# Kernel optimization log

Hardware: AMD Instinct MI355X
Metric: run time of the kernel (lower is better)

Reference implementation:

```python
import jax, jax.numpy as jnp
import numpy as np

B, T, D_IN, D_HID, D_OUT, N_CAT = 128, 64, 1024, 1024, 1536, 32


def setup_inputs() -> dict:
    key = jax.random.key(0)
    kx, kw1, kw2, kc = jax.random.split(key, 4)
    x = jax.random.normal(kx, (B, T, D_IN), dtype=jnp.float32)
    W1 = 0.02 * jax.random.normal(kw1, (N_CAT, D_IN, D_HID), dtype=jnp.float32)
    b1 = jnp.zeros((N_CAT, D_HID), dtype=jnp.float32)
    W2 = 0.02 * jax.random.normal(kw2, (N_CAT, D_HID, D_OUT), dtype=jnp.float32)
    b2 = jnp.zeros((N_CAT, D_OUT), dtype=jnp.float32)
    cat_ids = jax.random.randint(kc, (B,), 0, N_CAT)
    return {"x": x, "W1": W1, "b1": b1, "W2": W2, "b2": b2, "cat_ids": cat_ids}


def reference(x, W1, b1, W2, b2, cat_ids):
    # CategorySpecificLinear: gather per-sample expert weights, then batched matmul.
    # Layer 1: (B,T,D_in) @ (B,D_in,D_hid) + (B,1,D_hid)
    h = jnp.einsum('btd,bdh->bth', x, W1[cat_ids]) + b1[cat_ids][:, None, :]
    h = jax.nn.relu(h)
    # Layer 2: (B,T,D_hid) @ (B,D_hid,D_out) + (B,1,D_out)
    out = jnp.einsum('bth,bho->bto', h, W2[cat_ids]) + b2[cat_ids][:, None, :]
    return out
```

## Files before the change

kernel.cpp:

```cpp
#include <hip/hip_runtime.h>
#include <hip/hip_bf16.h>
#include <stdint.h>

#define NB    128
#define TT    64
#define KTOT  1024
#define DHID  1024
#define DOUT  1536
#define NCAT  32

#define BK    64
#define TN    128
#define PADR  72

typedef unsigned short u16;
typedef __attribute__((ext_vector_type(8))) short bf16x8;
typedef __attribute__((ext_vector_type(4))) float f32x4;
typedef __attribute__((ext_vector_type(4))) unsigned int uint4v;
typedef __attribute__((ext_vector_type(4))) float float4v;

__device__ __forceinline__ float bf2f(u16 u) {
    unsigned int x = ((unsigned int)u) << 16;
    return __builtin_bit_cast(float, x);
}
__device__ __forceinline__ unsigned int f2bf_u32(float f) {
    unsigned int x = __builtin_bit_cast(unsigned int, f);
    return (x + 0x7FFFu + ((x >> 16) & 1u)) >> 16;
}
__device__ __forceinline__ u16 f2bf(float f) { return (u16)f2bf_u32(f); }

__device__ int g_is_f32;

__global__ void detect_dtype(const unsigned int* __restrict__ xw) {
    if (threadIdx.x == 0 && blockIdx.x == 0) {
        int hits = 0;
        for (int i = 0; i < 256; ++i) {
            unsigned int e = (xw[i] >> 7) & 0xFF;
            hits += (e >= 120 && e <= 132) ? 1 : 0;
        }
        g_is_f32 = (hits < 128) ? 1 : 0;
    }
}

template<int NW, bool RELU, bool A_DYN, bool OUT_DYN>
__global__ __launch_bounds__(256, 4)
void gemm_cat(const void* __restrict__ Ain,
              const void* __restrict__ Win,
              const void* __restrict__ BiasIn,
              void* __restrict__ Cout,
              const int* __restrict__ cat_ids)
{
    constexpr int NT = NW / TN;
    __shared__ u16 As[TT * PADR];
    __shared__ u16 Bs[TN * PADR];

    const bool f32  = (g_is_f32 != 0);
    const bool aF32 = A_DYN && f32;
    const bool oF32 = OUT_DYN && f32;

    const int b   = blockIdx.x / NT;
    const int nt  = blockIdx.x % NT;
    const int cat = cat_ids[b];

    const int tid  = threadIdx.x;
    const int lane = tid & 63;
    const int l16  = lane & 15;
    const int q    = lane >> 4;
    const int wave = tid >> 6;
    const int wm   = wave & 1;
    const int wn   = wave >> 1;

    const size_t aOff = (size_t)b * (TT * KTOT);
    const u16*   Ab16 = (const u16*)Ain + aOff;
    const float* Ab32 = (const float*)Ain + aOff;
    const size_t wOff = (size_t)cat * ((size_t)KTOT * NW) + (size_t)nt * TN;
    const u16*   Wb16 = (const u16*)Win + wOff;
    const float* Wb32 = (const float*)Win + wOff;

    const int ar = tid >> 2;
    const int ac = (tid & 3) * 16;
    const int bn  = tid & 127;
    const int bk0 = tid >> 7;

    f32x4 acc[2][4];
#pragma unroll
    for (int im = 0; im < 2; ++im)
#pragma unroll
        for (int in = 0; in < 4; ++in)
            acc[im][in] = (f32x4){0.f, 0.f, 0.f, 0.f};

    for (int kk = 0; kk < KTOT; kk += BK) {
        if (!aF32) {
            const u16* src = Ab16 + ar * KTOT + kk + ac;
            uint4v v0 = *(const uint4v*)(src);
            uint4v v1 = *(const uint4v*)(src + 8);
            *(uint4v*)&As[ar * PADR + ac]     = v0;
            *(uint4v*)&As[ar * PADR + ac + 8] = v1;
        } else {
            const float* src = Ab32 + ar * KTOT + kk + ac;
            float4v f0 = *(const float4v*)(src);
            float4v f1 = *(const float4v*)(src + 4);
            float4v f2 = *(const float4v*)(src + 8);
            float4v f3 = *(const float4v*)(src + 12);
            uint4v v0, v1;
            v0.x = f2bf_u32(f0.x) | (f2bf_u32(f0.y) << 16);
            v0.y = f2bf_u32(f0.z) | (f2bf_u32(f0.w) << 16);
            v0.z = f2bf_u32(f1.x) | (f2bf_u32(f1.y) << 16);
            v0.w = f2bf_u32(f1.z) | (f2bf_u32(f1.w) << 16);
            v1.x = f2bf_u32(f2.x) | (f2bf_u32(f2.y) << 16);
            v1.y = f2bf_u32(f2.z) | (f2bf_u32(f2.w) << 16);
            v1.z = f2bf_u32(f3.x) | (f2bf_u32(f3.y) << 16);
            v1.w = f2bf_u32(f3.z) | (f2bf_u32(f3.w) << 16);
            *(uint4v*)&As[ar * PADR + ac]     = v0;
            *(uint4v*)&As[ar * PADR + ac + 8] = v1;
        }
#pragma unroll
        for (int i = 0; i < 4; ++i) {
            const int kc = bk0 + i * 2;
            unsigned int s[8];
            if (!f32) {
                const u16* src = Wb16 + (size_t)(kk + kc * 8) * NW + bn;
#pragma unroll
                for (int j = 0; j < 8; ++j) s[j] = src[(size_t)j * NW];
            } else {
                const float* src = Wb32 + (size_t)(kk + kc * 8) * NW + bn;
#pragma unroll
                for (int j = 0; j < 8; ++j) s[j] = f2bf_u32(src[(size_t)j * NW]);
            }
            uint4v v;
            v.x = s[0] | (s[1] << 16);
            v.y = s[2] | (s[3] << 16);
            v.z = s[4] | (s[5] << 16);
            v.w = s[6] | (s[7] << 16);
            *(uint4v*)&Bs[bn * PADR + kc * 8] = v;
        }
        __syncthreads();

#pragma unroll
        for (int s = 0; s < 2; ++s) {
            bf16x8 a[2], bb[4];
#pragma unroll
            for (int im = 0; im < 2; ++im)
                a[im] = *(const bf16x8*)&As[(wm * 32 + im * 16 + l16) * PADR + s * 32 + q * 8];
#pragma unroll
            for (int in = 0; in < 4; ++in)
                bb[in] = *(const bf16x8*)&Bs[(wn * 64 + in * 16 + l16) * PADR + s * 32 + q * 8];
#pragma unroll
            for (int im = 0; im < 2; ++im)
#pragma unroll
                for (int in = 0; in < 4; ++in)
                    acc[im][in] = __builtin_amdgcn_mfma_f32_16x16x32_bf16(
                        a[im], bb[in], acc[im][in], 0, 0, 0);
        }
        __syncthreads();
    }

    const u16*   bias16 = (const u16*)BiasIn + (size_t)cat * NW + nt * TN;
    const float* bias32 = (const float*)BiasIn + (size_t)cat * NW + nt * TN;
    const size_t cOff = (size_t)b * TT * NW + (size_t)nt * TN;
    u16*   C16 = (u16*)Cout + cOff;
    float* C32 = (float*)Cout + cOff;
#pragma unroll
    for (int in = 0; in < 4; ++in) {
        const int ncol = wn * 64 + in * 16 + l16;
        const float bv = f32 ? bias32[ncol] : bf2f(bias16[ncol]);
#pragma unroll
        for (int im = 0; im < 2; ++im) {
#pragma unroll
            for (int r = 0; r < 4; ++r) {
                const int m = wm * 32 + im * 16 + q * 4 + r;
                float v = acc[im][in][r] + bv;
                if (RELU) v = fmaxf(v, 0.f);
                if (oF32) C32[(size_t)m * NW + ncol] = v;
                else      C16[(size_t)m * NW + ncol] = f2bf(v);
            }
        }
    }
}

extern "C" void kernel_launch(void* const* d_in, const int* in_sizes, int n_in,
                              void* d_out, int out_size, void* d_ws, size_t ws_size,
                              hipStream_t stream) {
    const void* x   = d_in[0];
    const void* W1  = d_in[1];
    const void* b1  = d_in[2];
    const void* W2  = d_in[3];
    const void* b2  = d_in[4];
    const int*  cid = (const int*)d_in[5];

    u16* h = (u16*)d_ws;

    detect_dtype<<<1, 64, 0, stream>>>((const unsigned int*)x);
    gemm_cat<DHID, true,  true,  false><<<NB * (DHID / TN), 256, 0, stream>>>(
        x, W1, b1, (void*)h, cid);
    gemm_cat<DOUT, false, false, true ><<<NB * (DOUT / TN), 256, 0, stream>>>(
        (const void*)h, W2, b2, d_out, cid);
}
```

Before: 558.6 us.

## Group samples by category so each weight tile serves up to four batches

Adds a build_groups kernel that sorts samples by category into groups of up to four. A new 512-thread GEMM loads each expert weight tile once and reuses it across all samples in its group. Weight traffic and fp32-to-bf16 conversion per sample drop accordingly. The new path also pre-converts x to bf16 in a separate pass, double-buffers LDS with async global_load_lds for A and register prefetch for W, uses XOR swizzling and a remapped block order, and parallelises dtype detection with a ballot. It needs a larger workspace, launches padded idle blocks, and falls back to the old kernels if the workspace is too small.

```diff
diff --git a/kernel.cpp b/kernel.cpp
--- a/kernel.cpp
+++ b/kernel.cpp
@@ -1,5 +1,4 @@
 #include <hip/hip_runtime.h>
-#include <hip/hip_bf16.h>
 #include <stdint.h>
 
 #define NB    128
@@ -12,6 +11,7 @@
 #define BK    64
 #define TN    128
 #define PADR  72
+#define NGMAX 64
 
 typedef unsigned short u16;
 typedef __attribute__((ext_vector_type(8))) short bf16x8;
@@ -32,13 +32,233 @@
 __device__ int g_is_f32;
 
 __global__ void detect_dtype(const unsigned int* __restrict__ xw) {
-    if (threadIdx.x == 0 && blockIdx.x == 0) {
-        int hits = 0;
-        for (int i = 0; i < 256; ++i) {
-            unsigned int e = (xw[i] >> 7) & 0xFF;
-            hits += (e >= 120 && e <= 132) ? 1 : 0;
-        }
-        g_is_f32 = (hits < 128) ? 1 : 0;
+    const int lane = threadIdx.x;
+    const unsigned int w = xw[lane * 64];
+    const unsigned int e = (w >> 7) & 0xFF;
+    const unsigned long long m = __ballot(e >= 120 && e <= 132);
+    if (lane == 0) g_is_f32 = (__popcll(m) < 32) ? 1 : 0;
+}
+
+__device__ __forceinline__ void gload16(const void* g, void* l) {
+    __builtin_amdgcn_global_load_lds(
+        (const __attribute__((address_space(1))) void*)g,
+        (__attribute__((address_space(3))) void*)l, 16, 0, 0);
+}
+
+__global__ void prep_x(const void* __restrict__ x, u16* __restrict__ xb) {
+    const bool f32 = (g_is_f32 != 0);
+    const size_t base = ((size_t)blockIdx.x * 256 + threadIdx.x) * 8;
+    if (f32) {
+        const float* s = (const float*)x + base;
+        float4v f0 = *(const float4v*)s;
+        float4v f1 = *(const float4v*)(s + 4);
+        uint4v v;
+        v.x = f2bf_u32(f0.x) | (f2bf_u32(f0.y) << 16);
+        v.y = f2bf_u32(f0.z) | (f2bf_u32(f0.w) << 16);
+        v.z = f2bf_u32(f1.x) | (f2bf_u32(f1.y) << 16);
+        v.w = f2bf_u32(f1.z) | (f2bf_u32(f1.w) << 16);
+        *(uint4v*)&xb[base] = v;
+    } else {
+        *(uint4v*)&xb[base] = *(const uint4v*)((const u16*)x + base);
+    }
+}
+
+__global__ void build_groups(const int* __restrict__ cid,
+                             int* __restrict__ gcat, int* __restrict__ gbat) {
+    __shared__ int cl[NB];
+    __shared__ int cnt[NCAT], start[NCAT], gbase[NCAT];
+    __shared__ int sorted[NB];
+    const int t = threadIdx.x;
+    cl[t] = cid[t];
+    if (t < NGMAX) gcat[t] = -1;
+    gbat[t] = -1; gbat[NB + t] = -1;
+    __syncthreads();
+    if (t < NCAT) {
+        int c = 0;
+        for (int i = 0; i < NB; ++i) c += (cl[i] == t) ? 1 : 0;
+        cnt[t] = c;
+    }
+    __syncthreads();
+    if (t == 0) {
+        int s = 0, g = 0;
+        for (int c = 0; c < NCAT; ++c) {
+            start[c] = s; s += cnt[c];
+            gbase[c] = g; g += (cnt[c] + 3) >> 2;
+        }
+    }
+    __syncthreads();
+    {
+        const int myc = cl[t];
+        int r = 0;
+        for (int i = 0; i < t; ++i) r += (cl[i] == myc) ? 1 : 0;
+        sorted[start[myc] + r] = t;
+    }
+    __syncthreads();
+    if (t < NCAT) {
+        const int n = cnt[t], ng = (n + 3) >> 2;
+        for (int j = 0; j < ng; ++j) {
+            const int g = gbase[t] + j;
+            gcat[g] = t;
+            for (int k = 0; k < 4; ++k) {
+                const int idx = j * 4 + k;
+                gbat[g * 4 + k] = (idx < n) ? sorted[start[t] + idx] : -1;
+            }
+        }
+    }
+}
+
+template<int NW, bool RELU, bool OUT_DYN>
+__global__ __launch_bounds__(512, 4)
+void gemm_grp(const u16* __restrict__ A,
+              const void* __restrict__ Win,
+              const void* __restrict__ BiasIn,
+              void* __restrict__ Cout,
+              const int* __restrict__ gcat,
+              const int* __restrict__ gbat)
+{
+    constexpr int NT   = NW / TN;
+    constexpr int NTIL = KTOT / 32;
+    __shared__ __align__(16) u16 As[2][4 * TT * 32];
+    __shared__ __align__(16) u16 Bs[2][TN * 32];
+
+    const int nwg = NGMAX * NT;
+    int bid = blockIdx.x;
+    bid = (bid & 7) * (nwg >> 3) + (bid >> 3);
+    const int g   = bid / NT;
+    const int nt  = bid % NT;
+    const int cat = gcat[g];
+    if (cat < 0) return;
+
+    const bool f32 = (g_is_f32 != 0);
+    const int t    = threadIdx.x;
+    const int wave = t >> 6;
+    const int lane = t & 63;
+    const int l16  = lane & 15;
+    const int q    = lane >> 4;
+    const int wm   = wave & 1;
+    const int wn   = wave >> 1;
+
+    const int bslot[4] = { gbat[g*4+0], gbat[g*4+1], gbat[g*4+2], gbat[g*4+3] };
+
+    const int tt   = t & 255;
+    const int arow = tt >> 2;
+    const int asc  = (((tt & 3) ^ ((tt >> 2) & 3) ^ ((tt >> 4) & 3)) << 3);
+    const int ah   = wave >> 2;
+    const int sA0  = ah, sA1 = 2 + ah;
+    const u16* aG0 = (bslot[sA0] >= 0)
+        ? (A + (size_t)bslot[sA0] * (TT * KTOT) + (size_t)arow * KTOT + asc) : (const u16*)0;
+    const u16* aG1 = (bslot[sA1] >= 0)
+        ? (A + (size_t)bslot[sA1] * (TT * KTOT) + (size_t)arow * KTOT + asc) : (const u16*)0;
+
+    const int bn  = t & 127;
+    const int kc  = t >> 7;
+    const int wch = ((kc ^ (bn & 3) ^ ((bn >> 2) & 3)) << 4);
+    const size_t wOff = (size_t)cat * ((size_t)KTOT * NW) + (size_t)(kc * 8) * NW
+                        + (size_t)nt * TN + bn;
+    const float* w32 = (const float*)Win + wOff;
+    const u16*   w16 = (const u16*)Win + wOff;
+
+    const int CH = ((q ^ (l16 & 3) ^ ((l16 >> 2) & 3)) << 4);
+
+    f32x4 acc[4][2][2];
+#pragma unroll
+    for (int bt = 0; bt < 4; ++bt)
+#pragma unroll
+        for (int im = 0; im < 2; ++im)
+#pragma unroll
+            for (int in = 0; in < 2; ++in)
+                acc[bt][im][in] = (f32x4){0.f, 0.f, 0.f, 0.f};
+
+    unsigned int wr[8];
+
+    auto W_ISSUE = [&](int kk) {
+        if (f32) {
+            const float* ws = w32 + (size_t)kk * NW;
+#pragma unroll
+            for (int j = 0; j < 8; ++j)
+                wr[j] = __builtin_bit_cast(unsigned int, ws[(size_t)j * NW]);
+        } else {
+            const u16* ws = w16 + (size_t)kk * NW;
+#pragma unroll
+            for (int j = 0; j < 8; ++j) wr[j] = ws[(size_t)j * NW];
+        }
+    };
+    auto W_PACK = [&](int pb) {
+        unsigned int p[4];
+#pragma unroll
+        for (int i = 0; i < 4; ++i) {
+            unsigned int lo, hi;
+            if (f32) {
+                lo = f2bf_u32(__builtin_bit_cast(float, wr[2*i]));
+                hi = f2bf_u32(__builtin_bit_cast(float, wr[2*i+1]));
+            } else { lo = wr[2*i]; hi = wr[2*i+1]; }
+            p[i] = lo | (hi << 16);
+        }
+        uint4v v; v.x = p[0]; v.y = p[1]; v.z = p[2]; v.w = p[3];
+        *(uint4v*)((char*)&Bs[pb][0] + bn * 64 + wch) = v;
+    };
+    auto A_ISSUE = [&](int pb, int kk) {
+        char* ab = (char*)&As[pb][0] + wave * 1024;
+        if (aG0) gload16(aG0 + kk, ab);
+        if (aG1) gload16(aG1 + kk, ab + 8192);
+    };
+    auto COMPUTE = [&](int pb) {
+        const char* bsb = (const char*)&Bs[pb][0];
+        const int nrow = wn * 32 + l16;
+        bf16x8 bb0 = *(const bf16x8*)(bsb + nrow * 64 + CH);
+        bf16x8 bb1 = *(const bf16x8*)(bsb + (nrow + 16) * 64 + CH);
+        const char* asb = (const char*)&As[pb][0] + (wm * 32 + l16) * 64 + CH;
+#pragma unroll
+        for (int bt = 0; bt < 4; ++bt) {
+            bf16x8 a0 = *(const bf16x8*)(asb + bt * 4096);
+            bf16x8 a1 = *(const bf16x8*)(asb + bt * 4096 + 1024);
+            acc[bt][0][0] = __builtin_amdgcn_mfma_f32_16x16x32_bf16(a0, bb0, acc[bt][0][0], 0, 0, 0);
+            acc[bt][0][1] = __builtin_amdgcn_mfma_f32_16x16x32_bf16(a0, bb1, acc[bt][0][1], 0, 0, 0);
+            acc[bt][1][0] = __builtin_amdgcn_mfma_f32_16x16x32_bf16(a1, bb0, acc[bt][1][0], 0, 0, 0);
+            acc[bt][1][1] = __builtin_amdgcn_mfma_f32_16x16x32_bf16(a1, bb1, acc[bt][1][1], 0, 0, 0);
+        }
+    };
+
+    W_ISSUE(0);
+    A_ISSUE(0, 0);
+    W_PACK(0);
+    __syncthreads();
+
+#pragma unroll 2
+    for (int tl = 0; tl < NTIL; ++tl) {
+        const int cur = tl & 1;
+        if (tl + 1 < NTIL) {
+            W_ISSUE((tl + 1) * 32);
+            A_ISSUE(cur ^ 1, (tl + 1) * 32);
+        }
+        COMPUTE(cur);
+        if (tl + 1 < NTIL) W_PACK(cur ^ 1);
+        __syncthreads();
+    }
+
+    const float* bias32 = (const float*)BiasIn + (size_t)cat * NW + (size_t)nt * TN;
+    const u16*   bias16 = (const u16*)BiasIn + (size_t)cat * NW + (size_t)nt * TN;
+#pragma unroll
+    for (int in = 0; in < 2; ++in) {
+        const int ncol = wn * 32 + in * 16 + l16;
+        const float bv = f32 ? bias32[ncol] : bf2f(bias16[ncol]);
+#pragma unroll
+        for (int bt = 0; bt < 4; ++bt) {
+            const int b = bslot[bt];
+            if (b < 0) continue;
+            const size_t cOff = (size_t)b * (TT * NW) + (size_t)nt * TN + ncol;
+#pragma unroll
+            for (int im = 0; im < 2; ++im) {
+#pragma unroll
+                for (int r = 0; r < 4; ++r) {
+                    const int m = wm * 32 + im * 16 + q * 4 + r;
+                    float v = acc[bt][im][in][r] + bv;
+                    if (RELU) v = fmaxf(v, 0.f);
+                    if (OUT_DYN && f32) ((float*)Cout)[cOff + (size_t)m * NW] = v;
+                    else                ((u16*)Cout)[cOff + (size_t)m * NW] = f2bf(v);
+                }
+            }
+        }
     }
 }
 
@@ -188,11 +408,28 @@
     const void* b2  = d_in[4];
     const int*  cid = (const int*)d_in[5];
 
-    u16* h = (u16*)d_ws;
+    const size_t XB_BYTES = (size_t)NB * TT * KTOT * 2;
+    const size_t NEED = 2 * XB_BYTES + 4096;
 
     detect_dtype<<<1, 64, 0, stream>>>((const unsigned int*)x);
-    gemm_cat<DHID, true,  true,  false><<<NB * (DHID / TN), 256, 0, stream>>>(
-        x, W1, b1, (void*)h, cid);
-    gemm_cat<DOUT, false, false, true ><<<NB * (DOUT / TN), 256, 0, stream>>>(
-        (const void*)h, W2, b2, d_out, cid);
-}
+
+    if (ws_size >= NEED) {
+        u16* xb   = (u16*)d_ws;
+        u16* h    = (u16*)((char*)d_ws + XB_BYTES);
+        int* gcat = (int*)((char*)d_ws + 2 * XB_BYTES);
+        int* gbat = gcat + NGMAX;
+
+        prep_x<<<4096, 256, 0, stream>>>(x, xb);
+        build_groups<<<1, NB, 0, stream>>>(cid, gcat, gbat);
+        gemm_grp<DHID, true,  false><<<NGMAX * (DHID / TN), 512, 0, stream>>>(
+            xb, W1, b1, (void*)h, gcat, gbat);
+        gemm_grp<DOUT, false, true ><<<NGMAX * (DOUT / TN), 512, 0, stream>>>(
+            h, W2, b2, d_out, gcat, gbat);
+    } else {
+        u16* h = (u16*)d_ws;
+        gemm_cat<DHID, true,  true,  false><<<NB * (DHID / TN), 256, 0, stream>>>(
+            x, W1, b1, (void*)h, cid);
+        gemm_cat<DOUT, false, false, true ><<<NB * (DOUT / TN), 256, 0, stream>>>(
+            (const void*)h, W2, b2, d_out, cid);
+    }
+}
```

Measured after the change: 492.9 us. 1.13x faster.
